# Performance work log

Hardware: AMD Instinct MI355X
Metric: run time of the kernel (lower is better)

## Reference

```python
import jax, jax.numpy as jnp
import numpy as np

B, S, D = 2, 2048, 7168
R, H, VD = 1024, 16, 128
QK_HD = R // H            # 64, per-head latent q/k dim
SCALE = float(np.sqrt(D // H))  # self.scale = d_heads ** 0.5 = sqrt(448)


def setup_inputs() -> dict:
    key = jax.random.key(0)
    ks = jax.random.split(key, 6)
    return {
        "x":   jax.random.normal(ks[0], (B, S, D), dtype=jnp.float32),
        "Wq":  jax.random.normal(ks[1], (R, D), dtype=jnp.float32) * 0.02,
        "Wkv": jax.random.normal(ks[2], (R, D), dtype=jnp.float32) * 0.02,
        "Wvb": jax.random.normal(ks[3], (H * VD, R), dtype=jnp.float32) * 0.02,
        "Wo":  jax.random.normal(ks[4], (D, H * VD), dtype=jnp.float32) * 0.02,
        "bo":  jnp.zeros((D,), dtype=jnp.float32),
    }


def reference(x, Wq, Wkv, Wvb, Wo, bo):
    b, s, d = x.shape
    # low-rank compressed projections (torch Linear: y = x @ W.T)
    q_lat  = x @ Wq.T            # [B,S,R] compressed query
    kv_lat = x @ Wkv.T           # [B,S,R] compressed KV latent (shared K)
    q = q_lat.reshape(b, s, H, QK_HD)    # [B,S,H,64]
    k = kv_lat.reshape(b, s, H, QK_HD)   # [B,S,H,64]
    # up-project values from latent
    v = (kv_lat @ Wvb.T).reshape(b, s, H, VD)  # [B,S,H,128]
    # scaled causal attention in latent head space
    scores = jnp.einsum("bqhd,bkhd->bhqk", q, k) / SCALE  # [B,H,S,S]
    causal = jnp.tril(jnp.ones((s, s), dtype=bool))
    scores = jnp.where(causal, scores, jnp.finfo(scores.dtype).min)
    attn = jax.nn.softmax(scores, axis=-1)
    out = jnp.einsum("bhqk,bkhd->bqhd", attn, v).reshape(b, s, H * VD)
    return out @ Wo.T + bo       # [B,S,D]
```

## Files before the change

kernel.cpp:

```cpp
#include <hip/hip_runtime.h>
#include <hip/hip_bf16.h>

typedef __bf16 bf16_t;
typedef __attribute__((ext_vector_type(8))) __bf16 bf16x8;
typedef __attribute__((ext_vector_type(4))) __bf16 bf16x4;
typedef __attribute__((ext_vector_type(4))) float f32x4;

#define B_ 2
#define S_ 2048
#define D_ 7168
#define R_ 1024
#define H_ 16
#define VD_ 128
#define MROWS 4096
#define NQKV 2048
#define HVD 2048

__device__ __forceinline__ void gload_lds16(const bf16_t* g, bf16_t* l) {
    __builtin_amdgcn_global_load_lds(
        (const __attribute__((address_space(1))) unsigned int*)(g),
        (__attribute__((address_space(3))) unsigned int*)(l),
        16, 0, 0);
}

__global__ __launch_bounds__(256)
void cvt_fused(const float* __restrict__ x,  const float* __restrict__ Wq,
               const float* __restrict__ Wkv, const float* __restrict__ Wvb,
               const float* __restrict__ Wo,
               bf16_t* __restrict__ xb, bf16_t* __restrict__ Wqkv_b,
               bf16_t* __restrict__ Wvb_b, bf16_t* __restrict__ Wo_b,
               float inv_scale)
{
    const long c = ((long)blockIdx.x * 256 + threadIdx.x);
    const long e = c * 8;
    const float* src; bf16_t* dst; long off; float scale = 1.0f;
    if (e < 29360128L) {
        src = x;   dst = xb;              off = e;
    } else if (e < 36700160L) {
        src = Wq;  dst = Wqkv_b;          off = e - 29360128L; scale = inv_scale;
    } else if (e < 44040192L) {
        src = Wkv; dst = Wqkv_b + 7340032; off = e - 36700160L;
    } else if (e < 46137344L) {
        src = Wvb; dst = Wvb_b;           off = e - 44040192L;
    } else {
        src = Wo;  dst = Wo_b;            off = e - 46137344L;
    }
    f32x4 v0 = *(const f32x4*)(src + off);
    f32x4 v1 = *(const f32x4*)(src + off + 4);
    bf16x8 o;
    o[0] = (bf16_t)(v0[0] * scale); o[1] = (bf16_t)(v0[1] * scale);
    o[2] = (bf16_t)(v0[2] * scale); o[3] = (bf16_t)(v0[3] * scale);
    o[4] = (bf16_t)(v1[0] * scale); o[5] = (bf16_t)(v1[1] * scale);
    o[6] = (bf16_t)(v1[2] * scale); o[7] = (bf16_t)(v1[3] * scale);
    *(bf16x8*)(dst + off) = o;
}

template<int OUTF32>
__global__ __launch_bounds__(256)
void gemm_bt(const bf16_t* __restrict__ A, int lda,
             const bf16_t* __restrict__ Bt, int ldb,
             void* __restrict__ Cv, int ldc,
             const float* __restrict__ bias, int K)
{
    __shared__ __align__(16) bf16_t As[2][128 * 64];
    __shared__ __align__(16) bf16_t Bs[2][128 * 64];
    const int tid  = threadIdx.x;
    const int lane = tid & 63;
    const int wave = tid >> 6;
    const int tileM = blockIdx.y * 128;
    const int tileN = blockIdx.x * 128;
    const int wr = (wave >> 1) * 64;
    const int wc = (wave & 1) * 64;
    const int r  = lane & 15;
    const int kq = lane >> 4;

    const bf16_t* Ag = A  + (size_t)tileM * lda;
    const bf16_t* Bg = Bt + (size_t)tileN * ldb;

    int srow[4], scol[4], slin[4];
    #pragma unroll
    for (int i = 0; i < 4; ++i) {
        slin[i] = (i * 256 + tid) * 8;
        srow[i] = slin[i] >> 6;
        scol[i] = (slin[i] & 63) ^ ((srow[i] & 7) << 3);
    }

    #define ISSUE_TILE(buf, k0)                                                  \
        {                                                                        \
            _Pragma("unroll")                                                    \
            for (int i = 0; i < 4; ++i) {                                        \
                gload_lds16(Ag + (size_t)srow[i] * lda + (k0) + scol[i], As[buf] + slin[i]); \
                gload_lds16(Bg + (size_t)srow[i] * ldb + (k0) + scol[i], Bs[buf] + slin[i]); \
            }                                                                    \
        }

    f32x4 acc[4][4] = {};
    const int nt = K >> 6;

    ISSUE_TILE(0, 0)
    ISSUE_TILE(1, 64)
    asm volatile("s_waitcnt vmcnt(8)" ::: "memory");
    __builtin_amdgcn_s_barrier();
    __builtin_amdgcn_sched_barrier(0);

    for (int t = 0; t < nt; ++t) {
        const int cur = t & 1;
        const bf16_t* Ab = As[cur];
        const bf16_t* Bb = Bs[cur];

        bf16x8 af[4][2], bfr[4][2];
        #pragma unroll
        for (int m = 0; m < 4; ++m)
            #pragma unroll
            for (int kk = 0; kk < 2; ++kk) {
                const int e = (wr + m * 16 + r) * 64 + kk * 32 + kq * 8;
                af[m][kk] = *(const bf16x8*)(Ab + (e ^ ((r & 7) << 3)));
            }
        #pragma unroll
        for (int n = 0; n < 4; ++n)
            #pragma unroll
            for (int kk = 0; kk < 2; ++kk) {
                const int e = (wc + n * 16 + r) * 64 + kk * 32 + kq * 8;
                bfr[n][kk] = *(const bf16x8*)(Bb + (e ^ ((r & 7) << 3)));
            }
        __builtin_amdgcn_s_setprio(1);
        #pragma unroll
        for (int kk = 0; kk < 2; ++kk)
            #pragma unroll
            for (int m = 0; m < 4; ++m)
                #pragma unroll
                for (int n = 0; n < 4; ++n)
                    acc[m][n] = __builtin_amdgcn_mfma_f32_16x16x32_bf16(af[m][kk], bfr[n][kk], acc[m][n], 0, 0, 0);
        __builtin_amdgcn_s_setprio(0);

        __builtin_amdgcn_s_barrier();
        __builtin_amdgcn_sched_barrier(0);
        if (t + 2 < nt) {
            ISSUE_TILE(cur, (t + 2) << 6)
            asm volatile("s_waitcnt vmcnt(8)" ::: "memory");
        } else {
            asm volatile("s_waitcnt vmcnt(0)" ::: "memory");
        }
        __builtin_amdgcn_s_barrier();
        __builtin_amdgcn_sched_barrier(0);
    }
    #undef ISSUE_TILE

    const int orow = tileM + wr + kq * 4;
    const int ocol = tileN + wc + r;
    if (OUTF32) {
        float* C = (float*)Cv;
        #pragma unroll
        for (int n = 0; n < 4; ++n) {
            float bv = bias[ocol + n * 16];
            #pragma unroll
            for (int m = 0; m < 4; ++m)
                #pragma unroll
                for (int j = 0; j < 4; ++j)
                    C[(size_t)(orow + m * 16 + j) * ldc + ocol + n * 16] = acc[m][n][j] + bv;
        }
    } else {
        bf16_t* C = (bf16_t*)Cv;
        #pragma unroll
        for (int m = 0; m < 4; ++m)
            #pragma unroll
            for (int n = 0; n < 4; ++n)
                #pragma unroll
                for (int j = 0; j < 4; ++j)
                    C[(size_t)(orow + m * 16 + j) * ldc + ocol + n * 16] = (bf16_t)acc[m][n][j];
    }
}

template<int OUTF32>
__global__ __launch_bounds__(512, 2)
void gemm_bt256p(const bf16_t* __restrict__ A, int lda,
                 const bf16_t* __restrict__ Bt, int ldb,
                 void* __restrict__ Cv, int ldc,
                 const float* __restrict__ bias, int K)
{
    __shared__ __align__(16) bf16_t As[2][256 * 64];
    __shared__ __align__(16) bf16_t Bs[2][256 * 64];
    const int tid  = threadIdx.x;
    const int lane = tid & 63;
    const int wave = tid >> 6;
    const int wm = wave >> 2;
    const int wn = wave & 3;
    const int tileM = blockIdx.y * 256;
    const int tileN = blockIdx.x * 256;
    const int r  = lane & 15;
    const int kq = lane >> 4;

    const bf16_t* Ag = A  + (size_t)tileM * lda;
    const bf16_t* Bg = Bt + (size_t)tileN * ldb;

    int sr[2], sc[2], sl[2];
    #pragma unroll
    for (int i = 0; i < 2; ++i) {
        sl[i] = (i * 512 + tid) * 8;
        sr[i] = sl[i] >> 6;
        sc[i] = (sl[i] & 63) ^ ((sr[i] & 7) << 3);
    }

    #define STA(buf, k0, h)                                                      \
        { _Pragma("unroll")                                                      \
          for (int i = 0; i < 2; ++i)                                            \
              gload_lds16(Ag + (size_t)((h) * 128 + sr[i]) * lda + (k0) + sc[i], \
                          As[buf] + (h) * 8192 + sl[i]); }
    #define STB(buf, k0, h)                                                      \
        { _Pragma("unroll")                                                      \
          for (int i = 0; i < 2; ++i)                                            \
              gload_lds16(Bg + (size_t)((h) * 128 + sr[i]) * ldb + (k0) + sc[i], \
                          Bs[buf] + (h) * 8192 + sl[i]); }

    #define PHASE(buf, q, READB, STAGE_STMT, VM_STMT)                            \
        {                                                                        \
            const bf16_t* Ab_ = As[buf];                                         \
            const bf16_t* Bb_ = Bs[buf];                                         \
            bf16x8 af_[2][2];                                                    \
            _Pragma("unroll")                                                    \
            for (int mm = 0; mm < 2; ++mm)                                       \
                _Pragma("unroll")                                                \
                for (int kk = 0; kk < 2; ++kk) {                                 \
                    const int e = (wm * 128 + ((q) * 2 + mm) * 16 + r) * 64 + kk * 32 + kq * 8; \
                    af_[mm][kk] = *(const bf16x8*)(Ab_ + (e ^ ((r & 7) << 3)));  \
                }                                                                \
            if (READB) {                                                         \
                _Pragma("unroll")                                                \
                for (int n = 0; n < 4; ++n)                                      \
                    _Pragma("unroll")                                            \
                    for (int kk = 0; kk < 2; ++kk) {                             \
                        const int e = (wn * 64 + n * 16 + r) * 64 + kk * 32 + kq * 8; \
                        bf[n][kk] = *(const bf16x8*)(Bb_ + (e ^ ((r & 7) << 3))); \
                    }                                                            \
            }                                                                    \
            STAGE_STMT                                                           \
            VM_STMT                                                              \
            __builtin_amdgcn_s_barrier();                                        \
            asm volatile("s_waitcnt lgkmcnt(0)" ::: "memory");                   \
            __builtin_amdgcn_sched_barrier(0);                                   \
            __builtin_amdgcn_s_setprio(1);                                       \
            _Pragma("unroll")                                                    \
            for (int mm = 0; mm < 2; ++mm)                                       \
                _Pragma("unroll")                                                \
                for (int n = 0; n < 4; ++n)                                      \
                    _Pragma("unroll")                                            \
                    for (int kk = 0; kk < 2; ++kk)                               \
                        acc[(q) * 2 + mm][n] = __builtin_amdgcn_mfma_f32_16x16x32_bf16( \
                            af_[mm][kk], bf[n][kk], acc[(q) * 2 + mm][n], 0, 0, 0); \
            __builtin_amdgcn_s_setprio(0);                                       \
            __builtin_amdgcn_s_barrier();                                        \
            __builtin_amdgcn_sched_barrier(0);                                   \
        }

    f32x4 acc[8][4] = {};
    const int nt = K >> 6;
    const int niter = nt >> 1;

    STA(0, 0, 0) STA(0, 0, 1) STB(0, 0, 0) STB(0, 0, 1) STB(1, 64, 0) STB(1, 64, 1)
    asm volatile("s_waitcnt vmcnt(4)" ::: "memory");
    __builtin_amdgcn_s_barrier();
    __builtin_amdgcn_sched_barrier(0);

    for (int t = 0; t < niter; ++t) {
        const int k1 = (2 * t + 1) << 6;
        const int k2 = (2 * t + 2) << 6;
        const int k3 = (2 * t + 3) << 6;
        const bool more = (2 * t + 2) < nt;
        bf16x8 bf[4][2];

        PHASE(0, 0, 1, { STA(1, k1, 0) }, {})
        PHASE(0, 1, 0, { STA(1, k1, 1) }, {})
        PHASE(0, 2, 0, { if (more) STB(0, k2, 0) }, {})
        PHASE(0, 3, 0, { if (more) STB(0, k2, 1) },
              { if (more) { asm volatile("s_waitcnt vmcnt(4)" ::: "memory"); }
                else      { asm volatile("s_waitcnt vmcnt(0)" ::: "memory"); } })
        PHASE(1, 0, 1, { if (more) STA(0, k2, 0) }, {})
        PHASE(1, 1, 0, { if (more) STA(0, k2, 1) }, {})
        PHASE(1, 2, 0, { if (more) STB(1, k3, 0) }, {})
        PHASE(1, 3, 0, { if (more) STB(1, k3, 1) },
              { if (more) { asm volatile("s_waitcnt vmcnt(4)" ::: "memory"); } })
    }
    #undef PHASE
    #undef STA
    #undef STB

    const int orow = tileM + wm * 128 + kq * 4;
    const int ocol = tileN + wn * 64 + r;
    if (OUTF32) {
        float* C = (float*)Cv;
        #pragma unroll
        for (int n = 0; n < 4; ++n) {
            float bv = bias[ocol + n * 16];
            #pragma unroll
            for (int m = 0; m < 8; ++m)
                #pragma unroll
                for (int j = 0; j < 4; ++j)
                    C[(size_t)(orow + m * 16 + j) * ldc + ocol + n * 16] = acc[m][n][j] + bv;
        }
    } else {
        bf16_t* C = (bf16_t*)Cv;
        #pragma unroll
        for (int m = 0; m < 8; ++m)
            #pragma unroll
            for (int n = 0; n < 4; ++n)
                #pragma unroll
                for (int j = 0; j < 4; ++j)
                    C[(size_t)(orow + m * 16 + j) * ldc + ocol + n * 16] = (bf16_t)acc[m][n][j];
    }
}

__device__ __forceinline__ void attn_qtile(
    const bf16_t* __restrict__ Q, const bf16_t* __restrict__ Kp,
    const bf16_t* __restrict__ Vp, bf16_t* __restrict__ Op,
    bf16_t* __restrict__ P_lds, int qbase, int lane)
{
    const int r  = lane & 15;
    const int kq = lane >> 4;

    bf16x8 qf[2][2];
    #pragma unroll
    for (int m = 0; m < 2; ++m)
        #pragma unroll
        for (int kk = 0; kk < 2; ++kk)
            qf[m][kk] = *(const bf16x8*)(Q + (size_t)(qbase + m * 16 + r) * NQKV + kk * 32 + kq * 8);

    f32x4 o[2][8] = {};
    float mst[2][4], lst[2][4];
    #pragma unroll
    for (int m = 0; m < 2; ++m)
        #pragma unroll
        for (int j = 0; j < 4; ++j) { mst[m][j] = -INFINITY; lst[m][j] = 0.0f; }

    const int nfull  = qbase >> 6;
    const int ntiles = (qbase + 95) >> 6;

    for (int t = 0; t < ntiles; ++t) {
        const int kvb = t * 64;
        f32x4 s[2][4] = {};
        #pragma unroll
        for (int n = 0; n < 4; ++n) {
            bf16x8 kf0 = *(const bf16x8*)(Kp + (size_t)(kvb + n * 16 + r) * NQKV + kq * 8);
            bf16x8 kf1 = *(const bf16x8*)(Kp + (size_t)(kvb + n * 16 + r) * NQKV + 32 + kq * 8);
            #pragma unroll
            for (int m = 0; m < 2; ++m) {
                s[m][n] = __builtin_amdgcn_mfma_f32_16x16x32_bf16(qf[m][0], kf0, s[m][n], 0, 0, 0);
                s[m][n] = __builtin_amdgcn_mfma_f32_16x16x32_bf16(qf[m][1], kf1, s[m][n], 0, 0, 0);
            }
        }
        if (t >= nfull) {
            #pragma unroll
            for (int m = 0; m < 2; ++m)
                #pragma unroll
                for (int n = 0; n < 4; ++n)
                    #pragma unroll
                    for (int j = 0; j < 4; ++j) {
                        int kc = kvb + n * 16 + r;
                        int qr = qbase + m * 16 + kq * 4 + j;
                        if (kc > qr) s[m][n][j] = -1e30f;
                    }
        }
        float mx[2][4];
        #pragma unroll
        for (int m = 0; m < 2; ++m)
            #pragma unroll
            for (int j = 0; j < 4; ++j) {
                float v = fmaxf(fmaxf(s[m][0][j], s[m][1][j]), fmaxf(s[m][2][j], s[m][3][j]));
                #pragma unroll
                for (int d = 1; d < 16; d <<= 1) v = fmaxf(v, __shfl_xor(v, d, 64));
                mx[m][j] = v;
            }
        bool need = false;
        #pragma unroll
        for (int m = 0; m < 2; ++m)
            #pragma unroll
            for (int j = 0; j < 4; ++j) need |= (mx[m][j] > mst[m][j] + 8.0f);
        if (__ballot(need)) {
            #pragma unroll
            for (int m = 0; m < 2; ++m)
                #pragma unroll
                for (int j = 0; j < 4; ++j) {
                    float mnew  = fmaxf(mst[m][j], mx[m][j]);
                    float alpha = __expf(mst[m][j] - mnew);
                    lst[m][j] *= alpha;
                    mst[m][j]  = mnew;
                    #pragma unroll
                    for (int n = 0; n < 8; ++n) o[m][n][j] *= alpha;
                }
        }
        #pragma unroll
        for (int m = 0; m < 2; ++m)
            #pragma unroll
            for (int j = 0; j < 4; ++j) {
                float rs = 0.0f;
                const int row = m * 16 + kq * 4 + j;
                #pragma unroll
                for (int n = 0; n < 4; ++n) {
                    float pv = __expf(s[m][n][j] - mst[m][j]);
                    rs += pv;
                    const int c = (n * 16 + r) ^ ((row & 7) << 3);
                    P_lds[row * 64 + c] = (bf16_t)pv;
                }
                #pragma unroll
                for (int d = 1; d < 16; d <<= 1) rs += __shfl_xor(rs, d, 64);
                lst[m][j] += rs;
            }
        __syncthreads();
        bf16x8 pf[2][2];
        #pragma unroll
        for (int m = 0; m < 2; ++m)
            #pragma unroll
            for (int kk = 0; kk < 2; ++kk) {
                const int e = (m * 16 + r) * 64 + kk * 32 + kq * 8;
                pf[m][kk] = *(const bf16x8*)(P_lds + (e ^ ((r & 7) << 3)));
            }
        #pragma unroll
        for (int n = 0; n < 8; ++n) {
            #pragma unroll
            for (int kk = 0; kk < 2; ++kk) {
                bf16x8 vf = *(const bf16x8*)(Vp + (size_t)(n * 16 + r) * MROWS + kvb + kk * 32 + kq * 8);
                #pragma unroll
                for (int m = 0; m < 2; ++m)
                    o[m][n] = __builtin_amdgcn_mfma_f32_16x16x32_bf16(pf[m][kk], vf, o[m][n], 0, 0, 0);
            }
        }
        __syncthreads();
    }

    #pragma unroll
    for (int m = 0; m < 2; ++m)
        #pragma unroll
        for (int j = 0; j < 4; ++j) {
            float inv = 1.0f / lst[m][j];
            int row = m * 16 + kq * 4 + j;
            #pragma unroll
            for (int n = 0; n < 8; ++n)
                Op[(size_t)(qbase + row) * HVD + n * 16 + r] = (bf16_t)(o[m][n][j] * inv);
        }
}

__global__ __launch_bounds__(64)
void attn_kernel(const bf16_t* __restrict__ qkv, const bf16_t* __restrict__ Vt,
                 bf16_t* __restrict__ O)
{
    __shared__ __align__(16) bf16_t P_lds[32 * 64];
    const int lane = threadIdx.x;
    const int p = blockIdx.x;
    const int h = blockIdx.y;
    const int b = blockIdx.z;

    const bf16_t* Q  = qkv + (size_t)(b * S_) * NQKV + h * 64;
    const bf16_t* Kp = qkv + (size_t)(b * S_) * NQKV + R_ + h * 64;
    const bf16_t* Vp = Vt + (size_t)(h * VD_) * MROWS + b * S_;
    bf16_t* Op = O + (size_t)(b * S_) * HVD + h * VD_;

    attn_qtile(Q, Kp, Vp, Op, P_lds, (63 - p) * 32, lane);
    attn_qtile(Q, Kp, Vp, Op, P_lds, p * 32, lane);
}

extern "C" void kernel_launch(void* const* d_in, const int* in_sizes, int n_in,
                              void* d_out, int out_size, void* d_ws, size_t ws_size,
                              hipStream_t stream) {
    const float* x   = (const float*)d_in[0];
    const float* Wq  = (const float*)d_in[1];
    const float* Wkv = (const float*)d_in[2];
    const float* Wvb = (const float*)d_in[3];
    const float* Wo  = (const float*)d_in[4];
    const float* bo  = (const float*)d_in[5];

    char* oc = (char*)d_out;
    bf16_t* xb     = (bf16_t*)oc;
    bf16_t* Wqkv_b = (bf16_t*)(oc + 58720256);
    char* ws = (char*)d_ws;
    bf16_t* qkv_b  = (bf16_t*)ws;
    bf16_t* Wvb_b  = (bf16_t*)(ws + 16777216);
    bf16_t* Vt_b   = (bf16_t*)(ws + 20971520);
    bf16_t* attn_b = (bf16_t*)(ws + 37748736);
    bf16_t* Wo_b   = (bf16_t*)(ws + 54525952);

    const float inv_scale = 0.047245559f;

    cvt_fused<<<29696, 256, 0, stream>>>(x, Wq, Wkv, Wvb, Wo,
                                         xb, Wqkv_b, Wvb_b, Wo_b, inv_scale);

    gemm_bt<0><<<dim3(16, 32), 256, 0, stream>>>(xb, D_, Wqkv_b, D_, qkv_b, NQKV, nullptr, D_);
    gemm_bt<0><<<dim3(32, 16), 256, 0, stream>>>(Wvb_b, R_, qkv_b + R_, NQKV, Vt_b, MROWS, nullptr, R_);
    attn_kernel<<<dim3(32, H_, B_), 64, 0, stream>>>(qkv_b, Vt_b, attn_b);
    gemm_bt256p<1><<<dim3(28, 16), 512, 0, stream>>>(attn_b, HVD, Wo_b, HVD, d_out, D_, bo, HVD);
}
```

Baseline: 487.8 us.

## Process paired high and low query tiles in one fused KV loop

The attention kernel used to walk the KV sequence twice per block, once for the late query tile and once for the early one. It now runs a single loop over the high tile's KV range and also updates the low tile while its range is still active, so each K and V fragment loaded from global memory feeds both tiles. The cost is roughly double the register state (two sets of accumulators, Q fragments and softmax stats), with launch bounds set to one block per SIMD. That raises register pressure and may lower occupancy or cause spills.

```diff
diff --git a/kernel.cpp b/kernel.cpp
--- a/kernel.cpp
+++ b/kernel.cpp
@@ -309,141 +309,15 @@
     }
 }
 
-__device__ __forceinline__ void attn_qtile(
-    const bf16_t* __restrict__ Q, const bf16_t* __restrict__ Kp,
-    const bf16_t* __restrict__ Vp, bf16_t* __restrict__ Op,
-    bf16_t* __restrict__ P_lds, int qbase, int lane)
-{
-    const int r  = lane & 15;
-    const int kq = lane >> 4;
-
-    bf16x8 qf[2][2];
-    #pragma unroll
-    for (int m = 0; m < 2; ++m)
-        #pragma unroll
-        for (int kk = 0; kk < 2; ++kk)
-            qf[m][kk] = *(const bf16x8*)(Q + (size_t)(qbase + m * 16 + r) * NQKV + kk * 32 + kq * 8);
-
-    f32x4 o[2][8] = {};
-    float mst[2][4], lst[2][4];
-    #pragma unroll
-    for (int m = 0; m < 2; ++m)
-        #pragma unroll
-        for (int j = 0; j < 4; ++j) { mst[m][j] = -INFINITY; lst[m][j] = 0.0f; }
-
-    const int nfull  = qbase >> 6;
-    const int ntiles = (qbase + 95) >> 6;
-
-    for (int t = 0; t < ntiles; ++t) {
-        const int kvb = t * 64;
-        f32x4 s[2][4] = {};
-        #pragma unroll
-        for (int n = 0; n < 4; ++n) {
-            bf16x8 kf0 = *(const bf16x8*)(Kp + (size_t)(kvb + n * 16 + r) * NQKV + kq * 8);
-            bf16x8 kf1 = *(const bf16x8*)(Kp + (size_t)(kvb + n * 16 + r) * NQKV + 32 + kq * 8);
-            #pragma unroll
-            for (int m = 0; m < 2; ++m) {
-                s[m][n] = __builtin_amdgcn_mfma_f32_16x16x32_bf16(qf[m][0], kf0, s[m][n], 0, 0, 0);
-                s[m][n] = __builtin_amdgcn_mfma_f32_16x16x32_bf16(qf[m][1], kf1, s[m][n], 0, 0, 0);
-            }
-        }
-        if (t >= nfull) {
-            #pragma unroll
-            for (int m = 0; m < 2; ++m)
-                #pragma unroll
-                for (int n = 0; n < 4; ++n)
-                    #pragma unroll
-                    for (int j = 0; j < 4; ++j) {
-                        int kc = kvb + n * 16 + r;
-                        int qr = qbase + m * 16 + kq * 4 + j;
-                        if (kc > qr) s[m][n][j] = -1e30f;
-                    }
-        }
-        float mx[2][4];
-        #pragma unroll
-        for (int m = 0; m < 2; ++m)
-            #pragma unroll
-            for (int j = 0; j < 4; ++j) {
-                float v = fmaxf(fmaxf(s[m][0][j], s[m][1][j]), fmaxf(s[m][2][j], s[m][3][j]));
-                #pragma unroll
-                for (int d = 1; d < 16; d <<= 1) v = fmaxf(v, __shfl_xor(v, d, 64));
-                mx[m][j] = v;
-            }
-        bool need = false;
-        #pragma unroll
-        for (int m = 0; m < 2; ++m)
-            #pragma unroll
-            for (int j = 0; j < 4; ++j) need |= (mx[m][j] > mst[m][j] + 8.0f);
-        if (__ballot(need)) {
-            #pragma unroll
-            for (int m = 0; m < 2; ++m)
-                #pragma unroll
-                for (int j = 0; j < 4; ++j) {
-                    float mnew  = fmaxf(mst[m][j], mx[m][j]);
-                    float alpha = __expf(mst[m][j] - mnew);
-                    lst[m][j] *= alpha;
-                    mst[m][j]  = mnew;
-                    #pragma unroll
-                    for (int n = 0; n < 8; ++n) o[m][n][j] *= alpha;
-                }
-        }
-        #pragma unroll
-        for (int m = 0; m < 2; ++m)
-            #pragma unroll
-            for (int j = 0; j < 4; ++j) {
-                float rs = 0.0f;
-                const int row = m * 16 + kq * 4 + j;
-                #pragma unroll
-                for (int n = 0; n < 4; ++n) {
-                    float pv = __expf(s[m][n][j] - mst[m][j]);
-                    rs += pv;
-                    const int c = (n * 16 + r) ^ ((row & 7) << 3);
-                    P_lds[row * 64 + c] = (bf16_t)pv;
-                }
-                #pragma unroll
-                for (int d = 1; d < 16; d <<= 1) rs += __shfl_xor(rs, d, 64);
-                lst[m][j] += rs;
-            }
-        __syncthreads();
-        bf16x8 pf[2][2];
-        #pragma unroll
-        for (int m = 0; m < 2; ++m)
-            #pragma unroll
-            for (int kk = 0; kk < 2; ++kk) {
-                const int e = (m * 16 + r) * 64 + kk * 32 + kq * 8;
-                pf[m][kk] = *(const bf16x8*)(P_lds + (e ^ ((r & 7) << 3)));
-            }
-        #pragma unroll
-        for (int n = 0; n < 8; ++n) {
-            #pragma unroll
-            for (int kk = 0; kk < 2; ++kk) {
-                bf16x8 vf = *(const bf16x8*)(Vp + (size_t)(n * 16 + r) * MROWS + kvb + kk * 32 + kq * 8);
-                #pragma unroll
-                for (int m = 0; m < 2; ++m)
-                    o[m][n] = __builtin_amdgcn_mfma_f32_16x16x32_bf16(pf[m][kk], vf, o[m][n], 0, 0, 0);
-            }
-        }
-        __syncthreads();
-    }
-
-    #pragma unroll
-    for (int m = 0; m < 2; ++m)
-        #pragma unroll
-        for (int j = 0; j < 4; ++j) {
-            float inv = 1.0f / lst[m][j];
-            int row = m * 16 + kq * 4 + j;
-            #pragma unroll
-            for (int n = 0; n < 8; ++n)
-                Op[(size_t)(qbase + row) * HVD + n * 16 + r] = (bf16_t)(o[m][n][j] * inv);
-        }
-}
-
-__global__ __launch_bounds__(64)
+__global__ __launch_bounds__(64, 1)
 void attn_kernel(const bf16_t* __restrict__ qkv, const bf16_t* __restrict__ Vt,
                  bf16_t* __restrict__ O)
 {
-    __shared__ __align__(16) bf16_t P_lds[32 * 64];
+    __shared__ __align__(16) bf16_t P_h[32 * 64];
+    __shared__ __align__(16) bf16_t P_l[32 * 64];
     const int lane = threadIdx.x;
+    const int r  = lane & 15;
+    const int kq = lane >> 4;
     const int p = blockIdx.x;
     const int h = blockIdx.y;
     const int b = blockIdx.z;
@@ -453,8 +327,206 @@
     const bf16_t* Vp = Vt + (size_t)(h * VD_) * MROWS + b * S_;
     bf16_t* Op = O + (size_t)(b * S_) * HVD + h * VD_;
 
-    attn_qtile(Q, Kp, Vp, Op, P_lds, (63 - p) * 32, lane);
-    attn_qtile(Q, Kp, Vp, Op, P_lds, p * 32, lane);
+    const int qb_h = (63 - p) * 32;
+    const int qb_l = p * 32;
+
+    bf16x8 qfh[2][2], qfl[2][2];
+    #pragma unroll
+    for (int m = 0; m < 2; ++m)
+        #pragma unroll
+        for (int kk = 0; kk < 2; ++kk) {
+            qfh[m][kk] = *(const bf16x8*)(Q + (size_t)(qb_h + m * 16 + r) * NQKV + kk * 32 + kq * 8);
+            qfl[m][kk] = *(const bf16x8*)(Q + (size_t)(qb_l + m * 16 + r) * NQKV + kk * 32 + kq * 8);
+        }
+
+    f32x4 oh[2][8] = {}, ol[2][8] = {};
+    float msh[2][4], lsh[2][4], msl[2][4], lsl[2][4];
+    #pragma unroll
+    for (int m = 0; m < 2; ++m)
+        #pragma unroll
+        for (int j = 0; j < 4; ++j) {
+            msh[m][j] = -INFINITY; lsh[m][j] = 0.0f;
+            msl[m][j] = -INFINITY; lsl[m][j] = 0.0f;
+        }
+
+    const int nfull_h = qb_h >> 6, ntiles_h = (qb_h + 95) >> 6;
+    const int nfull_l = qb_l >> 6, ntiles_l = (qb_l + 95) >> 6;
+
+    for (int t = 0; t < ntiles_h; ++t) {
+        const int kvb = t * 64;
+        const bool dol = (t < ntiles_l);
+
+        bf16x8 kf[4][2];
+        #pragma unroll
+        for (int n = 0; n < 4; ++n) {
+            const bf16_t* kp = Kp + (size_t)(kvb + n * 16 + r) * NQKV + kq * 8;
+            kf[n][0] = *(const bf16x8*)kp;
+            kf[n][1] = *(const bf16x8*)(kp + 32);
+        }
+        f32x4 sh[2][4] = {}, sl_[2][4] = {};
+        #pragma unroll
+        for (int n = 0; n < 4; ++n)
+            #pragma unroll
+            for (int m = 0; m < 2; ++m) {
+                sh[m][n] = __builtin_amdgcn_mfma_f32_16x16x32_bf16(qfh[m][0], kf[n][0], sh[m][n], 0, 0, 0);
+                sh[m][n] = __builtin_amdgcn_mfma_f32_16x16x32_bf16(qfh[m][1], kf[n][1], sh[m][n], 0, 0, 0);
+            }
+        if (dol) {
+            #pragma unroll
+            for (int n = 0; n < 4; ++n)
+                #pragma unroll
+                for (int m = 0; m < 2; ++m) {
+                    sl_[m][n] = __builtin_amdgcn_mfma_f32_16x16x32_bf16(qfl[m][0], kf[n][0], sl_[m][n], 0, 0, 0);
+                    sl_[m][n] = __builtin_amdgcn_mfma_f32_16x16x32_bf16(qfl[m][1], kf[n][1], sl_[m][n], 0, 0, 0);
+                }
+        }
+        if (t >= nfull_h) {
+            #pragma unroll
+            for (int m = 0; m < 2; ++m)
+                #pragma unroll
+                for (int n = 0; n < 4; ++n)
+                    #pragma unroll
+                    for (int j = 0; j < 4; ++j) {
+                        int kc = kvb + n * 16 + r;
+                        int qr = qb_h + m * 16 + kq * 4 + j;
+                        if (kc > qr) sh[m][n][j] = -1e30f;
+                    }
+        }
+        if (dol && t >= nfull_l) {
+            #pragma unroll
+            for (int m = 0; m < 2; ++m)
+                #pragma unroll
+                for (int n = 0; n < 4; ++n)
+                    #pragma unroll
+                    for (int j = 0; j < 4; ++j) {
+                        int kc = kvb + n * 16 + r;
+                        int qr = qb_l + m * 16 + kq * 4 + j;
+                        if (kc > qr) sl_[m][n][j] = -1e30f;
+                    }
+        }
+        float mxh[2][4], mxl[2][4];
+        #pragma unroll
+        for (int m = 0; m < 2; ++m)
+            #pragma unroll
+            for (int j = 0; j < 4; ++j) {
+                float v = fmaxf(fmaxf(sh[m][0][j], sh[m][1][j]), fmaxf(sh[m][2][j], sh[m][3][j]));
+                #pragma unroll
+                for (int d = 1; d < 16; d <<= 1) v = fmaxf(v, __shfl_xor(v, d, 64));
+                mxh[m][j] = v;
+            }
+        if (dol) {
+            #pragma unroll
+            for (int m = 0; m < 2; ++m)
+                #pragma unroll
+                for (int j = 0; j < 4; ++j) {
+                    float v = fmaxf(fmaxf(sl_[m][0][j], sl_[m][1][j]), fmaxf(sl_[m][2][j], sl_[m][3][j]));
+                    #pragma unroll
+                    for (int d = 1; d < 16; d <<= 1) v = fmaxf(v, __shfl_xor(v, d, 64));
+                    mxl[m][j] = v;
+                }
+        }
+        bool needh = false, needl = false;
+        #pragma unroll
+        for (int m = 0; m < 2; ++m)
+            #pragma unroll
+            for (int j = 0; j < 4; ++j) {
+                needh |= (mxh[m][j] > msh[m][j] + 8.0f);
+                if (dol) needl |= (mxl[m][j] > msl[m][j] + 8.0f);
+            }
+        if (__ballot(needh)) {
+            #pragma unroll
+            for (int m = 0; m < 2; ++m)
+                #pragma unroll
+                for (int j = 0; j < 4; ++j) {
+                    float mnew  = fmaxf(msh[m][j], mxh[m][j]);
+                    float alpha = __expf(msh[m][j] - mnew);
+                    lsh[m][j] *= alpha;
+                    msh[m][j]  = mnew;
+                    #pragma unroll
+                    for (int n = 0; n < 8; ++n) oh[m][n][j] *= alpha;
+                }
+        }
+        if (dol && __ballot(needl)) {
+            #pragma unroll
+            for (int m = 0; m < 2; ++m)
+                #pragma unroll
+                for (int j = 0; j < 4; ++j) {
+                    float mnew  = fmaxf(msl[m][j], mxl[m][j]);
+                    float alpha = __expf(msl[m][j] - mnew);
+                    lsl[m][j] *= alpha;
+                    msl[m][j]  = mnew;
+                    #pragma unroll
+                    for (int n = 0; n < 8; ++n) ol[m][n][j] *= alpha;
+                }
+        }
+        #pragma unroll
+        for (int m = 0; m < 2; ++m)
+            #pragma unroll
+            for (int j = 0; j < 4; ++j) {
+                const int row = m * 16 + kq * 4 + j;
+                float rsh = 0.0f;
+                #pragma unroll
+                for (int n = 0; n < 4; ++n) {
+                    float pv = __expf(sh[m][n][j] - msh[m][j]);
+                    rsh += pv;
+                    const int c = (n * 16 + r) ^ ((row & 7) << 3);
+                    P_h[row * 64 + c] = (bf16_t)pv;
+                }
+                #pragma unroll
+                for (int d = 1; d < 16; d <<= 1) rsh += __shfl_xor(rsh, d, 64);
+                lsh[m][j] += rsh;
+                if (dol) {
+                    float rsl = 0.0f;
+                    #pragma unroll
+                    for (int n = 0; n < 4; ++n) {
+                        float pv = __expf(sl_[m][n][j] - msl[m][j]);
+                        rsl += pv;
+                        const int c = (n * 16 + r) ^ ((row & 7) << 3);
+                        P_l[row * 64 + c] = (bf16_t)pv;
+                    }
+                    #pragma unroll
+                    for (int d = 1; d < 16; d <<= 1) rsl += __shfl_xor(rsl, d, 64);
+                    lsl[m][j] += rsl;
+                }
+            }
+        __syncthreads();
+        bf16x8 pfh[2][2], pfl[2][2];
+        #pragma unroll
+        for (int m = 0; m < 2; ++m)
+            #pragma unroll
+            for (int kk = 0; kk < 2; ++kk) {
+                const int e = (m * 16 + r) * 64 + kk * 32 + kq * 8;
+                pfh[m][kk] = *(const bf16x8*)(P_h + (e ^ ((r & 7) << 3)));
+                if (dol) pfl[m][kk] = *(const bf16x8*)(P_l + (e ^ ((r & 7) << 3)));
+            }
+        #pragma unroll
+        for (int n = 0; n < 8; ++n) {
+            #pragma unroll
+            for (int kk = 0; kk < 2; ++kk) {
+                bf16x8 vf = *(const bf16x8*)(Vp + (size_t)(n * 16 + r) * MROWS + kvb + kk * 32 + kq * 8);
+                #pragma unroll
+                for (int m = 0; m < 2; ++m) {
+                    oh[m][n] = __builtin_amdgcn_mfma_f32_16x16x32_bf16(pfh[m][kk], vf, oh[m][n], 0, 0, 0);
+                    if (dol) ol[m][n] = __builtin_amdgcn_mfma_f32_16x16x32_bf16(pfl[m][kk], vf, ol[m][n], 0, 0, 0);
+                }
+            }
+        }
+        __syncthreads();
+    }
+
+    #pragma unroll
+    for (int m = 0; m < 2; ++m)
+        #pragma unroll
+        for (int j = 0; j < 4; ++j) {
+            const int row = m * 16 + kq * 4 + j;
+            float invh = 1.0f / lsh[m][j];
+            float invl = 1.0f / lsl[m][j];
+            #pragma unroll
+            for (int n = 0; n < 8; ++n) {
+                Op[(size_t)(qb_h + row) * HVD + n * 16 + r] = (bf16_t)(oh[m][n][j] * invh);
+                Op[(size_t)(qb_l + row) * HVD + n * 16 + r] = (bf16_t)(ol[m][n][j] * invl);
+            }
+        }
 }
 
 extern "C" void kernel_launch(void* const* d_in, const int* in_sizes, int n_in,
```

Measured after the change: 631.6 us. 1.29x slower.
